# Optimization experiments

Measured on AMD Instinct MI355X. Metric: run time of the kernel, lower is better.

Reference implementation:

```python
import jax, jax.numpy as jnp
import numpy as np

N_NODES = 50000
N_EDGES = 1600000
D = 128
L = 4
N_GRAPHS = 512


def setup_inputs() -> dict:
    key = jax.random.key(0)
    ks = jax.random.split(key, 8)
    x = jax.random.normal(ks[0], (N_NODES, D), dtype=jnp.float32)
    edge_index = jax.random.randint(ks[1], (2, N_EDGES), 0, N_NODES, dtype=jnp.int64)
    batch = jnp.sort(jax.random.randint(ks[2], (N_NODES,), 0, N_GRAPHS, dtype=jnp.int64))
    # MLP params per GIN layer: Linear(D->D), ReLU, Linear(D->D). Stacked over L layers.
    s = 1.0 / np.sqrt(D)
    Ws1 = jax.random.uniform(ks[3], (L, D, D), jnp.float32, -s, s)
    bs1 = jax.random.uniform(ks[4], (L, D), jnp.float32, -s, s)
    Ws2 = jax.random.uniform(ks[5], (L, D, D), jnp.float32, -s, s)
    bs2 = jax.random.uniform(ks[6], (L, D), jnp.float32, -s, s)
    return {"x": x, "edge_index": edge_index, "batch": batch,
            "Ws1": Ws1, "bs1": bs1, "Ws2": Ws2, "bs2": bs2}


def reference(x, edge_index, batch, Ws1, bs1, Ws2, bs2):
    src, dst = edge_index[0], edge_index[1]
    for l in range(L):
        # GINConv (eps=0): h = MLP(x + sum_{j in N(i)} x_j)
        agg = jax.ops.segment_sum(x[src], dst, num_segments=N_NODES)  # [N, D]
        h = x + agg
        h = jax.nn.relu(h @ Ws1[l] + bs1[l])
        x = h @ Ws2[l] + bs2[l]
    # global_add_pool: segment-sum node features by graph id
    return jax.ops.segment_sum(x, batch, num_segments=N_GRAPHS)  # [G, D]
```

## Files before the change

kernel.cpp:

```cpp
#include <hip/hip_runtime.h>

#define NN 50000
#define NE 1600000
#define DD 128
#define NL 4
#define NG 512
#define BSH 7
#define BMSK 127
#define NBUK 391
#define NBLK 196
#define EPB 8192
#define HN (NBUK * NBLK)
#define HT 150
#define EPT 20

typedef __attribute__((ext_vector_type(8))) short short8;
typedef __attribute__((ext_vector_type(4))) float floatx4;

__device__ __forceinline__ unsigned short f2bf(float f) {
    unsigned int u = __float_as_uint(f);
    u += 0x7fffu + ((u >> 16) & 1u);
    return (unsigned short)(u >> 16);
}
__device__ __forceinline__ float bf2f(unsigned short u) {
    return __uint_as_float(((unsigned int)u) << 16);
}

__global__ __launch_bounds__(256) void cvt_kernel(const float* __restrict__ x,
                                                  unsigned short* __restrict__ xbf) {
    int idx = blockIdx.x * 256 + threadIdx.x;
    float4 f = ((const float4*)x)[idx];
    ushort4 o;
    o.x = f2bf(f.x); o.y = f2bf(f.y); o.z = f2bf(f.z); o.w = f2bf(f.w);
    ((ushort4*)xbf)[idx] = o;
}


__global__ __launch_bounds__(512) void bhist_kernel(const int* __restrict__ dst,
                                                    int* __restrict__ hist) {
    __shared__ int h[NBUK];
    int tid = threadIdx.x;
    for (int i = tid; i < NBUK; i += 512) h[i] = 0;
    __syncthreads();
    int base = blockIdx.x * EPB;
#pragma unroll
    for (int it = 0; it < EPB / 512; it++) {
        int e = base + it * 512 + tid;
        if (e < NE) atomicAdd(&h[dst[e] >> BSH], 1);
    }
    __syncthreads();
    for (int i = tid; i < NBUK; i += 512) hist[i * NBLK + blockIdx.x] = h[i];
}

__global__ __launch_bounds__(512) void sum_tiles_kernel(const int* __restrict__ in,
                                                        int* __restrict__ tsum, int n) {
    int i = blockIdx.x * 512 + threadIdx.x;
    __shared__ int s[512];
    s[threadIdx.x] = (i < n) ? in[i] : 0;
    __syncthreads();
    for (int off = 256; off > 0; off >>= 1) {
        if (threadIdx.x < off) s[threadIdx.x] += s[threadIdx.x + off];
        __syncthreads();
    }
    if (threadIdx.x == 0) tsum[blockIdx.x] = s[0];
}

__global__ __launch_bounds__(256) void scan_tiles_kernel(const int* __restrict__ tsum,
                                                         int* __restrict__ toff, int ntiles) {
    int t = threadIdx.x;
    __shared__ int s[256];
    int v = (t < ntiles) ? tsum[t] : 0;
    s[t] = v;
    __syncthreads();
    for (int off = 1; off < 256; off <<= 1) {
        int u = (t >= off) ? s[t - off] : 0;
        __syncthreads();
        s[t] += u;
        __syncthreads();
    }
    if (t < ntiles) toff[t] = s[t] - v;
}

__global__ __launch_bounds__(512) void scan_out_kernel(const int* __restrict__ in,
                                                       const int* __restrict__ toff,
                                                       int* __restrict__ out, int n) {
    int i = blockIdx.x * 512 + threadIdx.x;
    int t = threadIdx.x;
    int v = (i < n) ? in[i] : 0;
    __shared__ int s[512];
    s[t] = v;
    __syncthreads();
    for (int off = 1; off < 512; off <<= 1) {
        int u = (t >= off) ? s[t - off] : 0;
        __syncthreads();
        s[t] += u;
        __syncthreads();
    }
    if (i < n) out[i] = toff[blockIdx.x] + s[t] - v;
}

__global__ __launch_bounds__(512) void bscatter_kernel(const int* __restrict__ src,
                                                       const int* __restrict__ dst,
                                                       const int* __restrict__ bkoff,
                                                       int* __restrict__ ebuf) {
    __shared__ int h[NBUK];
    int tid = threadIdx.x;
    for (int i = tid; i < NBUK; i += 512) h[i] = 0;
    __syncthreads();
    int base = blockIdx.x * EPB;
#pragma unroll
    for (int it = 0; it < EPB / 512; it++) {
        int e = base + it * 512 + tid;
        if (e < NE) {
            int d = dst[e];
            int bu = d >> BSH;
            int p = atomicAdd(&h[bu], 1);
            ebuf[bkoff[bu * NBLK + blockIdx.x] + p] = (src[e] << BSH) | (d & BMSK);
        }
    }
}

__global__ __launch_bounds__(256) void bucket_csr_kernel(const int* __restrict__ ebuf,
                                                         const int* __restrict__ bkoff,
                                                         int* __restrict__ rowptr,
                                                         int* __restrict__ rowend,
                                                         int* __restrict__ col) {
    __shared__ int cnt[128], exc[128], ebase[128];
    int b = blockIdx.x, tid = threadIdx.x;
    int segstart = bkoff[b * NBLK];
    int segend = (b < NBUK - 1) ? bkoff[(b + 1) * NBLK] : NE;
    if (tid < 128) cnt[tid] = 0;
    __syncthreads();
    int evr[EPT];
    int rnk[EPT];
#pragma unroll
    for (int j = 0; j < EPT; j++) {
        int i = segstart + tid + j * 256;
        if (i < segend) {
            int ev = ebuf[i];
            evr[j] = ev;
            rnk[j] = atomicAdd(&cnt[ev & BMSK], 1);
        } else {
            evr[j] = -1;
        }
    }
    __syncthreads();
    int v = (tid < 128) ? cnt[tid] : 0;
    if (tid < 128) exc[tid] = v;
    __syncthreads();
    for (int off = 1; off < 128; off <<= 1) {
        int u = (tid < 128 && tid >= off) ? exc[tid - off] : 0;
        __syncthreads();
        if (tid < 128) exc[tid] += u;
        __syncthreads();
    }
    if (tid < 128) {
        int excl = exc[tid] - v;
        ebase[tid] = segstart + excl;
        int node = (b << BSH) + tid;
        if (node < NN) {
            rowptr[node] = segstart + excl;
            rowend[node] = segstart + excl + v;
        }
    }
    __syncthreads();
#pragma unroll
    for (int j = 0; j < EPT; j++) {
        if (evr[j] >= 0) {
            int low = evr[j] & BMSK;
            col[ebase[low] + rnk[j]] = ((unsigned)evr[j]) >> BSH;
        }
    }
}

__global__ __launch_bounds__(256) void prep_kernel(const float* __restrict__ Ws1,
                                                   const float* __restrict__ Ws2,
                                                   unsigned short* __restrict__ W1T,
                                                   unsigned short* __restrict__ W2T) {
    int idx = blockIdx.x * 256 + threadIdx.x;
    int l = idx >> 14;
    int rem = idx & 16383;
    int k = rem >> 7;
    int n = rem & 127;
    int o = (l << 14) + (n << 7) + k;
    W1T[o] = f2bf(Ws1[idx]);
    W2T[o] = f2bf(Ws2[idx]);
}

__global__ __launch_bounds__(256) void agg_kernel(const unsigned short* __restrict__ xbf,
                                                  const int* __restrict__ rowptr,
                                                  const int* __restrict__ rowend,
                                                  const int* __restrict__ col,
                                                  unsigned short* __restrict__ hpre) {
    int g = threadIdx.x >> 4;
    int lane = threadIdx.x & 15;
    int node = blockIdx.x * 16 + g;
    const uint4* base = (const uint4*)xbf;
    float a[8];
    {
        uint4 v = base[node * 16 + lane];
        a[0] = __uint_as_float(v.x << 16); a[1] = __uint_as_float(v.x & 0xFFFF0000u);
        a[2] = __uint_as_float(v.y << 16); a[3] = __uint_as_float(v.y & 0xFFFF0000u);
        a[4] = __uint_as_float(v.z << 16); a[5] = __uint_as_float(v.z & 0xFFFF0000u);
        a[6] = __uint_as_float(v.w << 16); a[7] = __uint_as_float(v.w & 0xFFFF0000u);
    }
    int s = rowptr[node], e = rowend[node];
    int i = s;
    for (; i + 8 <= e; i += 8) {
        uint4 v0 = base[col[i] * 16 + lane];
        uint4 v1 = base[col[i + 1] * 16 + lane];
        uint4 v2 = base[col[i + 2] * 16 + lane];
        uint4 v3 = base[col[i + 3] * 16 + lane];
        uint4 v4 = base[col[i + 4] * 16 + lane];
        uint4 v5 = base[col[i + 5] * 16 + lane];
        uint4 v6 = base[col[i + 6] * 16 + lane];
        uint4 v7 = base[col[i + 7] * 16 + lane];
#define ACC(V)                                                            \
        a[0] += __uint_as_float(V.x << 16); a[1] += __uint_as_float(V.x & 0xFFFF0000u); \
        a[2] += __uint_as_float(V.y << 16); a[3] += __uint_as_float(V.y & 0xFFFF0000u); \
        a[4] += __uint_as_float(V.z << 16); a[5] += __uint_as_float(V.z & 0xFFFF0000u); \
        a[6] += __uint_as_float(V.w << 16); a[7] += __uint_as_float(V.w & 0xFFFF0000u)
        ACC(v0); ACC(v1); ACC(v2); ACC(v3); ACC(v4); ACC(v5); ACC(v6); ACC(v7);
    }
    for (; i < e; i++) {
        uint4 v = base[col[i] * 16 + lane];
        ACC(v);
    }
#undef ACC
    uint4 o;
    o.x = (unsigned int)f2bf(a[0]) | ((unsigned int)f2bf(a[1]) << 16);
    o.y = (unsigned int)f2bf(a[2]) | ((unsigned int)f2bf(a[3]) << 16);
    o.z = (unsigned int)f2bf(a[4]) | ((unsigned int)f2bf(a[5]) << 16);
    o.w = (unsigned int)f2bf(a[6]) | ((unsigned int)f2bf(a[7]) << 16);
    ((uint4*)hpre)[node * 16 + lane] = o;
}

__global__ __launch_bounds__(256) void mlp_kernel(const unsigned short* __restrict__ A,
                                                  const unsigned short* __restrict__ W1,
                                                  const float* __restrict__ b1,
                                                  const unsigned short* __restrict__ W2,
                                                  const float* __restrict__ b2,
                                                  unsigned short* __restrict__ O) {
    __shared__ unsigned short Wl[128 * 128];
    __shared__ unsigned short Hl[128 * 128];
    int tid = threadIdx.x;
    int wg = tid >> 6;
    int lane = tid & 63;
    int quad = lane >> 4;
    int li = lane & 15;
    int mg = wg >> 1, ng = wg & 1;
    int rowb = blockIdx.x * 128;

    {
        const uint4* wgl = (const uint4*)W1;
#pragma unroll
        for (int it = 0; it < 8; it++) {
            int idx = it * 256 + tid;
            int n = idx >> 4, kc = idx & 15;
            *(uint4*)&Wl[n * 128 + ((kc * 8) ^ ((n & 7) << 3))] = wgl[idx];
        }
    }
    __syncthreads();

    floatx4 acc[4][4];
#pragma unroll
    for (int tn = 0; tn < 4; tn++)
#pragma unroll
        for (int mi = 0; mi < 4; mi++) acc[tn][mi] = (floatx4){0.f, 0.f, 0.f, 0.f};

#pragma unroll
    for (int kk = 0; kk < 4; kk++) {
        int kc = kk * 32 + quad * 8;
        short8 xf[4];
#pragma unroll
        for (int mi = 0; mi < 4; mi++) {
            int ar = rowb + mg * 64 + mi * 16 + li;
            xf[mi] = (ar < NN) ? *(const short8*)(A + (size_t)ar * DD + kc)
                               : (short8){0, 0, 0, 0, 0, 0, 0, 0};
        }
#pragma unroll
        for (int tn = 0; tn < 4; tn++) {
            int wr = ng * 64 + tn * 16 + li;
            short8 wf = *(const short8*)&Wl[wr * 128 + (kc ^ ((wr & 7) << 3))];
#pragma unroll
            for (int mi = 0; mi < 4; mi++)
                acc[tn][mi] = __builtin_amdgcn_mfma_f32_16x16x32_bf16(wf, xf[mi], acc[tn][mi], 0, 0, 0);
        }
    }

#pragma unroll
    for (int tn = 0; tn < 4; tn++) {
        float4 bv = ((const float4*)b1)[ng * 16 + tn * 4 + quad];
#pragma unroll
        for (int mi = 0; mi < 4; mi++) {
            int hr = mg * 64 + mi * 16 + li;
            float v0 = fmaxf(acc[tn][mi][0] + bv.x, 0.f);
            float v1 = fmaxf(acc[tn][mi][1] + bv.y, 0.f);
            float v2 = fmaxf(acc[tn][mi][2] + bv.z, 0.f);
            float v3 = fmaxf(acc[tn][mi][3] + bv.w, 0.f);
            uint2 u;
            u.x = (unsigned int)f2bf(v0) | ((unsigned int)f2bf(v1) << 16);
            u.y = (unsigned int)f2bf(v2) | ((unsigned int)f2bf(v3) << 16);
            int c = (ng * 64 + tn * 16 + quad * 4) ^ ((hr & 7) << 3);
            *(uint2*)&Hl[hr * 128 + c] = u;
        }
    }
    __syncthreads();

    {
        const uint4* wgl = (const uint4*)W2;
#pragma unroll
        for (int it = 0; it < 8; it++) {
            int idx = it * 256 + tid;
            int n = idx >> 4, kc = idx & 15;
            *(uint4*)&Wl[n * 128 + ((kc * 8) ^ ((n & 7) << 3))] = wgl[idx];
        }
    }
    __syncthreads();

#pragma unroll
    for (int tn = 0; tn < 4; tn++)
#pragma unroll
        for (int mi = 0; mi < 4; mi++) acc[tn][mi] = (floatx4){0.f, 0.f, 0.f, 0.f};

#pragma unroll
    for (int kk = 0; kk < 4; kk++) {
        int kc = kk * 32 + quad * 8;
        short8 hf[4];
#pragma unroll
        for (int mi = 0; mi < 4; mi++) {
            int hr = mg * 64 + mi * 16 + li;
            hf[mi] = *(const short8*)&Hl[hr * 128 + (kc ^ ((hr & 7) << 3))];
        }
#pragma unroll
        for (int tn = 0; tn < 4; tn++) {
            int wr = ng * 64 + tn * 16 + li;
            short8 wf = *(const short8*)&Wl[wr * 128 + (kc ^ ((wr & 7) << 3))];
#pragma unroll
            for (int mi = 0; mi < 4; mi++)
                acc[tn][mi] = __builtin_amdgcn_mfma_f32_16x16x32_bf16(wf, hf[mi], acc[tn][mi], 0, 0, 0);
        }
    }

#pragma unroll
    for (int tn = 0; tn < 4; tn++) {
        float4 bv = ((const float4*)b2)[ng * 16 + tn * 4 + quad];
#pragma unroll
        for (int mi = 0; mi < 4; mi++) {
            int m = rowb + mg * 64 + mi * 16 + li;
            if (m < NN) {
                uint2 u;
                u.x = (unsigned int)f2bf(acc[tn][mi][0] + bv.x) |
                      ((unsigned int)f2bf(acc[tn][mi][1] + bv.y) << 16);
                u.y = (unsigned int)f2bf(acc[tn][mi][2] + bv.z) |
                      ((unsigned int)f2bf(acc[tn][mi][3] + bv.w) << 16);
                *(uint2*)&O[(size_t)m * DD + ng * 64 + tn * 16 + quad * 4] = u;
            }
        }
    }
}

__global__ __launch_bounds__(128) void pool_kernel(const unsigned short* __restrict__ x,
                                                   const int* __restrict__ batch,
                                                   float* __restrict__ out) {
    int g = blockIdx.x;
    int lo = 0, hi = NN;
    while (lo < hi) { int mid = (lo + hi) >> 1; if (batch[mid] < g) lo = mid + 1; else hi = mid; }
    int s = lo;
    hi = NN;
    while (lo < hi) { int mid = (lo + hi) >> 1; if (batch[mid] < g + 1) lo = mid + 1; else hi = mid; }
    int e = lo;
    int d = threadIdx.x;
    float acc = 0.f;
    for (int i = s; i < e; i++) acc += bf2f(x[(size_t)i * DD + d]);
    out[g * DD + d] = acc;
}

extern "C" void kernel_launch(void* const* d_in, const int* in_sizes, int n_in,
                              void* d_out, int out_size, void* d_ws, size_t ws_size,
                              hipStream_t stream) {
    const float* x0 = (const float*)d_in[0];
    const int* edge = (const int*)d_in[1];
    const int* batch = (const int*)d_in[2];
    const float* Ws1 = (const float*)d_in[3];
    const float* bs1 = (const float*)d_in[4];
    const float* Ws2 = (const float*)d_in[5];
    const float* bs2 = (const float*)d_in[6];
    float* out = (float*)d_out;
    const int* src = edge;
    const int* dst = edge + NE;

    char* ws = (char*)d_ws;
    size_t off = 0;
    auto alloc = [&](size_t bytes) {
        void* p = ws + off;
        off += (bytes + 255) & ~(size_t)255;
        return p;
    };
    unsigned short* x0bf = (unsigned short*)alloc((size_t)NN * DD * 2);
    unsigned short* xA = (unsigned short*)alloc((size_t)NN * DD * 2);
    unsigned short* xB = (unsigned short*)alloc((size_t)NN * DD * 2);
    unsigned short* hpre = (unsigned short*)alloc((size_t)NN * DD * 2);
    int* col = (int*)alloc((size_t)NE * 4);
    int* ebuf = (int*)alloc((size_t)NE * 4);
    int* hist = (int*)alloc((size_t)HN * 4);
    int* bkoff = (int*)alloc((size_t)HN * 4);
    int* tsum = (int*)alloc((size_t)HT * 4);
    int* toff = (int*)alloc((size_t)HT * 4);
    int* rowptr = (int*)alloc((size_t)(NN + 1) * 4);
    int* rowend = (int*)alloc((size_t)NN * 4);
    unsigned short* W1T = (unsigned short*)alloc((size_t)NL * DD * DD * 2);
    unsigned short* W2T = (unsigned short*)alloc((size_t)NL * DD * DD * 2);

    cvt_kernel<<<(NN * DD / 4) / 256, 256, 0, stream>>>(x0, x0bf);
    bhist_kernel<<<NBLK, 512, 0, stream>>>(dst, hist);
    sum_tiles_kernel<<<HT, 512, 0, stream>>>(hist, tsum, HN);
    scan_tiles_kernel<<<1, 256, 0, stream>>>(tsum, toff, HT);
    scan_out_kernel<<<HT, 512, 0, stream>>>(hist, toff, bkoff, HN);
    bscatter_kernel<<<NBLK, 512, 0, stream>>>(src, dst, bkoff, ebuf);
    bucket_csr_kernel<<<NBUK, 256, 0, stream>>>(ebuf, bkoff, rowptr, rowend, col);
    prep_kernel<<<(NL * DD * DD) / 256, 256, 0, stream>>>(Ws1, Ws2, W1T, W2T);

    const unsigned short* xin = x0bf;
    unsigned short* bufs[2] = {xA, xB};
    const int mlp_grid = (NN + 127) / 128;
    for (int l = 0; l < NL; l++) {
        agg_kernel<<<NN / 16, 256, 0, stream>>>(xin, rowptr, rowend, col, hpre);
        unsigned short* xout = bufs[l & 1];
        mlp_kernel<<<mlp_grid, 256, 0, stream>>>(hpre, W1T + l * DD * DD, bs1 + l * DD,
                                                 W2T + l * DD * DD, bs2 + l * DD, xout);
        xin = xout;
    }
    pool_kernel<<<NG, 128, 0, stream>>>(xin, batch, out);
}
```

Measured before the change: 436.3 us.

## Pre-sort edges by source bucket before destination bucketing for gather locality

Adds a first radix pass that buckets edges by source node (histogram, scan, scatter into a packed dst<<16|src buffer), then runs the existing destination-bucket pass over that buffer. Because the destination pass is stable within each block, neighbor lists in the CSR end up roughly ordered by source. The aim is more cache locality in the per-layer aggregation gathers. The cost is an extra histogram, scan and scatter pass over all edges, plus a 16-bit packing that only works because node ids fit below 65536.

```diff
diff --git a/kernel.cpp b/kernel.cpp
--- a/kernel.cpp
+++ b/kernel.cpp
@@ -36,7 +36,7 @@
 }
 
 
-__global__ __launch_bounds__(512) void bhist_kernel(const int* __restrict__ dst,
+__global__ __launch_bounds__(512) void shist_kernel(const int* __restrict__ src,
                                                     int* __restrict__ hist) {
     __shared__ int h[NBUK];
     int tid = threadIdx.x;
@@ -46,7 +46,7 @@
 #pragma unroll
     for (int it = 0; it < EPB / 512; it++) {
         int e = base + it * 512 + tid;
-        if (e < NE) atomicAdd(&h[dst[e] >> BSH], 1);
+        if (e < NE) atomicAdd(&h[src[e] >> BSH], 1);
     }
     __syncthreads();
     for (int i = tid; i < NBUK; i += 512) hist[i * NBLK + blockIdx.x] = h[i];
@@ -99,8 +99,45 @@
     if (i < n) out[i] = toff[blockIdx.x] + s[t] - v;
 }
 
-__global__ __launch_bounds__(512) void bscatter_kernel(const int* __restrict__ src,
+__global__ __launch_bounds__(512) void sscatter_kernel(const int* __restrict__ src,
                                                        const int* __restrict__ dst,
+                                                       const int* __restrict__ soff,
+                                                       unsigned int* __restrict__ ebufA) {
+    __shared__ int h[NBUK];
+    int tid = threadIdx.x;
+    for (int i = tid; i < NBUK; i += 512) h[i] = 0;
+    __syncthreads();
+    int base = blockIdx.x * EPB;
+#pragma unroll
+    for (int it = 0; it < EPB / 512; it++) {
+        int e = base + it * 512 + tid;
+        if (e < NE) {
+            int s = src[e];
+            int ss = s >> BSH;
+            int p = atomicAdd(&h[ss], 1);
+            ebufA[soff[ss * NBLK + blockIdx.x] + p] =
+                ((unsigned int)dst[e] << 16) | (unsigned int)s;
+        }
+    }
+}
+
+__global__ __launch_bounds__(512) void bhist_kernel(const unsigned int* __restrict__ ebufA,
+                                                    int* __restrict__ hist) {
+    __shared__ int h[NBUK];
+    int tid = threadIdx.x;
+    for (int i = tid; i < NBUK; i += 512) h[i] = 0;
+    __syncthreads();
+    int base = blockIdx.x * EPB;
+#pragma unroll
+    for (int it = 0; it < EPB / 512; it++) {
+        int e = base + it * 512 + tid;
+        if (e < NE) atomicAdd(&h[ebufA[e] >> (16 + BSH)], 1);
+    }
+    __syncthreads();
+    for (int i = tid; i < NBUK; i += 512) hist[i * NBLK + blockIdx.x] = h[i];
+}
+
+__global__ __launch_bounds__(512) void bscatter_kernel(const unsigned int* __restrict__ ebufA,
                                                        const int* __restrict__ bkoff,
                                                        int* __restrict__ ebuf) {
     __shared__ int h[NBUK];
@@ -112,10 +149,12 @@
     for (int it = 0; it < EPB / 512; it++) {
         int e = base + it * 512 + tid;
         if (e < NE) {
-            int d = dst[e];
+            unsigned int pk = ebufA[e];
+            int d = pk >> 16;
+            int s = pk & 0xFFFF;
             int bu = d >> BSH;
             int p = atomicAdd(&h[bu], 1);
-            ebuf[bkoff[bu * NBLK + blockIdx.x] + p] = (src[e] << BSH) | (d & BMSK);
+            ebuf[bkoff[bu * NBLK + blockIdx.x] + p] = (s << BSH) | (d & BMSK);
         }
     }
 }
@@ -403,8 +442,10 @@
     unsigned short* hpre = (unsigned short*)alloc((size_t)NN * DD * 2);
     int* col = (int*)alloc((size_t)NE * 4);
     int* ebuf = (int*)alloc((size_t)NE * 4);
+    unsigned int* ebufA = (unsigned int*)alloc((size_t)NE * 4);
     int* hist = (int*)alloc((size_t)HN * 4);
     int* bkoff = (int*)alloc((size_t)HN * 4);
+    int* soff = (int*)alloc((size_t)HN * 4);
     int* tsum = (int*)alloc((size_t)HT * 4);
     int* toff = (int*)alloc((size_t)HT * 4);
     int* rowptr = (int*)alloc((size_t)(NN + 1) * 4);
@@ -413,11 +454,16 @@
     unsigned short* W2T = (unsigned short*)alloc((size_t)NL * DD * DD * 2);
 
     cvt_kernel<<<(NN * DD / 4) / 256, 256, 0, stream>>>(x0, x0bf);
-    bhist_kernel<<<NBLK, 512, 0, stream>>>(dst, hist);
+    shist_kernel<<<NBLK, 512, 0, stream>>>(src, hist);
+    sum_tiles_kernel<<<HT, 512, 0, stream>>>(hist, tsum, HN);
+    scan_tiles_kernel<<<1, 256, 0, stream>>>(tsum, toff, HT);
+    scan_out_kernel<<<HT, 512, 0, stream>>>(hist, toff, soff, HN);
+    sscatter_kernel<<<NBLK, 512, 0, stream>>>(src, dst, soff, ebufA);
+    bhist_kernel<<<NBLK, 512, 0, stream>>>(ebufA, hist);
     sum_tiles_kernel<<<HT, 512, 0, stream>>>(hist, tsum, HN);
     scan_tiles_kernel<<<1, 256, 0, stream>>>(tsum, toff, HT);
     scan_out_kernel<<<HT, 512, 0, stream>>>(hist, toff, bkoff, HN);
-    bscatter_kernel<<<NBLK, 512, 0, stream>>>(src, dst, bkoff, ebuf);
+    bscatter_kernel<<<NBLK, 512, 0, stream>>>(ebufA, bkoff, ebuf);
     bucket_csr_kernel<<<NBUK, 256, 0, stream>>>(ebuf, bkoff, rowptr, rowend, col);
     prep_kernel<<<(NL * DD * DD) / 256, 256, 0, stream>>>(Ws1, Ws2, W1T, W2T);
 
```

Result: slower. 453.3 us (+3.9%).
